# Kernel optimization log

Measured on AMD Instinct MI355X. Metric: run time of the kernel, lower is better.

Reference implementation:

```python
import jax, jax.numpy as jnp
import numpy as np

TEMP = 0.07
W00 = 0.1
EPS = 1e-8


def setup_inputs() -> dict:
    key = jax.random.key(0)
    k1, k2, k3, k4 = jax.random.split(key, 4)
    B, N, D = 32, 256, 256
    M = B * N
    return {
        "audio_feats": jax.random.normal(k1, (B, N, D), dtype=jnp.float32),
        "visual_feats": jax.random.normal(k2, (B, N, D), dtype=jnp.float32),
        "audio_labels": jax.random.randint(k3, (M,), 0, 2, dtype=jnp.int64)
            if jax.config.jax_enable_x64 else jax.random.randint(k3, (M,), 0, 2, dtype=jnp.int32),
        "visual_labels": jax.random.randint(k4, (M,), 0, 2, dtype=jnp.int64)
            if jax.config.jax_enable_x64 else jax.random.randint(k4, (M,), 0, 2, dtype=jnp.int32),
    }


def reference(audio_feats, visual_feats, audio_labels, visual_labels):
    B, N, D = audio_feats.shape
    M = B * N
    a = audio_feats.reshape(M, D)
    v = visual_feats.reshape(M, D)
    # L2 normalize (torch F.normalize uses eps=1e-12 clamp on norm)
    a = a / jnp.maximum(jnp.linalg.norm(a, axis=-1, keepdims=True), 1e-12)
    v = v / jnp.maximum(jnp.linalg.norm(v, axis=-1, keepdims=True), 1e-12)
    sim = (a @ v.T) / TEMP  # (M, M)
    exp_sim = jnp.exp(sim)
    la = audio_labels[:, None]  # (M, 1)
    lv = visual_labels[None, :]  # (1, M)
    pos_mask = (la == lv) & ((la == 1) | (la == 0))
    weight = jnp.where(la == 1, 1.0, W00) * pos_mask.astype(sim.dtype)  # (M, M)
    wexp = exp_sim * weight

    # audio -> visual (row direction)
    denom_a2v = exp_sim.sum(axis=1)
    num_a2v = wexp.sum(axis=1)
    frac_a2v = (num_a2v + EPS) / (denom_a2v + EPS)
    valid_a2v = (num_a2v > 0).astype(sim.dtype)
    loss_a2v = -(valid_a2v * jnp.log(frac_a2v)).sum() / jnp.maximum(valid_a2v.sum(), 1.0)

    # visual -> audio (column direction)
    denom_v2a = exp_sim.sum(axis=0)
    num_v2a = wexp.sum(axis=0)
    frac_v2a = (num_v2a + EPS) / (denom_v2a + EPS)
    valid_v2a = (num_v2a > 0).astype(sim.dtype)
    loss_v2a = -(valid_v2a * jnp.log(frac_v2a)).sum() / jnp.maximum(valid_v2a.sum(), 1.0)

    return 0.5 * (loss_a2v + loss_v2a)
```

## Files before the change

kernel.cpp:

```cpp
#include <hip/hip_runtime.h>

#define M_ROWS 8192
#define D_DIM  256
#define BM     128
#define BN     64
#define NBI    (M_ROWS / BM)
#define NBJ    (M_ROWS / BN)
#define NJOBS  (NBI * NBJ)

#define ALPHA  4.53982478f


typedef __attribute__((ext_vector_type(4))) float floatx4;
typedef __attribute__((ext_vector_type(8))) int   intx8;

__device__ inline float fast_exp2(float x) {
#if __has_builtin(__builtin_amdgcn_exp2f)
    return __builtin_amdgcn_exp2f(x);
#else
    return exp2f(x);
#endif
}

__device__ inline floatx4 mfma_fp8(intx8 a, intx8 b, floatx4 c) {
    return __builtin_amdgcn_mfma_scale_f32_16x16x128_f8f6f4(
        a, b, c, 0, 0, 0, 0x7f7f7f7f, 0, 0x7f7f7f7f);
}

__global__ __launch_bounds__(256) void normalize_kernel(
    const float* __restrict__ af, const float* __restrict__ vf,
    unsigned char* __restrict__ aB, unsigned char* __restrict__ vB,
    float* __restrict__ glob)
{
    __shared__ float ssb[16][4];

    if (blockIdx.x == 0) {
        if (threadIdx.x < 4) glob[threadIdx.x] = 0.f;
        if (threadIdx.x == 4) ((int*)glob)[4] = 0;
    }

    const int b = blockIdx.x;
    const bool isA = b < 512;
    const int T = isA ? b : b - 512;
    const float* src = (isA ? af : vf) + (size_t)T * 16 * D_DIM;
    unsigned char* dst = (isA ? aB : vB) + (size_t)T * 4096;

    const int t    = threadIdx.x;
    const int wave = t >> 6, lane = t & 63;
    const int row  = t & 15;
    const int kq   = (t >> 4) & 3;
    const int h    = (t >> 6) & 1;
    const int s    = t >> 7;
    const int kbase = s * 128 + kq * 32 + h * 16;

    const float* p = src + row * D_DIM + kbase;
    float4 x0 = ((const float4*)p)[0], x1 = ((const float4*)p)[1];
    float4 x2 = ((const float4*)p)[2], x3 = ((const float4*)p)[3];

    float ss = x0.x*x0.x + x0.y*x0.y + x0.z*x0.z + x0.w*x0.w
             + x1.x*x1.x + x1.y*x1.y + x1.z*x1.z + x1.w*x1.w
             + x2.x*x2.x + x2.y*x2.y + x2.z*x2.z + x2.w*x2.w
             + x3.x*x3.x + x3.y*x3.y + x3.z*x3.z + x3.w*x3.w;
    ss += __shfl_xor(ss, 16, 64);
    ss += __shfl_xor(ss, 32, 64);
    if (lane < 16) ssb[lane][wave] = ss;
    __syncthreads();
    float tot = ssb[row][0] + ssb[row][1] + ssb[row][2] + ssb[row][3];
    float scale = ALPHA / fmaxf(sqrtf(tot), 1e-12f);

    int4 o;
    int pk;
    pk  = __builtin_amdgcn_cvt_pk_fp8_f32(x0.x*scale, x0.y*scale, 0, false);
    pk  = __builtin_amdgcn_cvt_pk_fp8_f32(x0.z*scale, x0.w*scale, pk, true);
    o.x = pk;
    pk  = __builtin_amdgcn_cvt_pk_fp8_f32(x1.x*scale, x1.y*scale, 0, false);
    pk  = __builtin_amdgcn_cvt_pk_fp8_f32(x1.z*scale, x1.w*scale, pk, true);
    o.y = pk;
    pk  = __builtin_amdgcn_cvt_pk_fp8_f32(x2.x*scale, x2.y*scale, 0, false);
    pk  = __builtin_amdgcn_cvt_pk_fp8_f32(x2.z*scale, x2.w*scale, pk, true);
    o.z = pk;
    pk  = __builtin_amdgcn_cvt_pk_fp8_f32(x3.x*scale, x3.y*scale, 0, false);
    pk  = __builtin_amdgcn_cvt_pk_fp8_f32(x3.z*scale, x3.w*scale, pk, true);
    o.w = pk;
    *(int4*)(dst + (size_t)t * 16) = o;
}

__global__ __launch_bounds__(256, 4) void gemm_loss_kernel(
    const unsigned char* __restrict__ aB, const unsigned char* __restrict__ vB,
    const int* __restrict__ la, const int* __restrict__ lv,
    float* __restrict__ rowPart, float* __restrict__ colPart)
{
    __shared__ unsigned char ldsB[16384];
    __shared__ float rowbuf[2 * BM];
    __shared__ float colbuf[8 * BN];

    const int tid  = threadIdx.x;
    const int wave = tid >> 6, lane = tid & 63;
    const int quad = lane >> 4, l16 = lane & 15;

    const int bx = blockIdx.x & 63;
    const int by = blockIdx.x >> 6;
    const int i0 = bx * BM, j0 = by * BN;

    {
        const unsigned char* vsrc = vB + (size_t)by * 16384 + (size_t)tid * 16;
        unsigned char* ldst = ldsB + tid * 16;
        #pragma unroll
        for (int c = 0; c < 4; ++c)
            *(int4*)(ldst + c * 4096) = *(const int4*)(vsrc + c * 4096);
    }

    const unsigned char* Abase = aB + (size_t)(bx * 8 + wave * 2) * 4096
                                    + (size_t)lane * 16;
    intx8 afr[2][2];
    #pragma unroll
    for (int it = 0; it < 2; ++it) {
        #pragma unroll
        for (int s = 0; s < 2; ++s) {
            int4 h0 = *(const int4*)(Abase + it * 4096 + s * 2048);
            int4 h1 = *(const int4*)(Abase + it * 4096 + s * 2048 + 1024);
            afr[it][s] = intx8{h0.x, h0.y, h0.z, h0.w, h1.x, h1.y, h1.z, h1.w};
        }
    }

    __syncthreads();

    floatx4 acc[2][4] = {};
    const unsigned char* Bl = ldsB + lane * 16;
    #pragma unroll
    for (int s = 0; s < 2; ++s) {
        #pragma unroll
        for (int jt = 0; jt < 4; ++jt) {
            int4 h0 = *(const int4*)(Bl + jt * 4096 + s * 2048);
            int4 h1 = *(const int4*)(Bl + jt * 4096 + s * 2048 + 1024);
            intx8 bf = intx8{h0.x, h0.y, h0.z, h0.w, h1.x, h1.y, h1.z, h1.w};
            acc[0][jt] = mfma_fp8(afr[0][s], bf, acc[0][jt]);
            acc[1][jt] = mfma_fp8(afr[1][s], bf, acc[1][jt]);
        }
    }

    const int baseRow = i0 + wave * 32;
    float maf[2][4];
    #pragma unroll
    for (int it = 0; it < 2; ++it)
        #pragma unroll
        for (int r = 0; r < 4; ++r)
            maf[it][r] = (float)la[baseRow + it * 16 + quad * 4 + r];
    float mvf[4];
    #pragma unroll
    for (int jt = 0; jt < 4; ++jt)
        mvf[jt] = (float)lv[j0 + jt * 16 + l16];

    float rT[2][4] = {}, r1[2][4] = {};
    float cT[4] = {}, c1[4] = {};
    #pragma unroll
    for (int it = 0; it < 2; ++it) {
        #pragma unroll
        for (int jt = 0; jt < 4; ++jt) {
            #pragma unroll
            for (int r = 0; r < 4; ++r) {
                float e = fast_exp2(acc[it][jt][r]);
                rT[it][r] += e;
                r1[it][r] = fmaf(mvf[jt], e, r1[it][r]);
                cT[jt] += e;
                c1[jt] = fmaf(maf[it][r], e, c1[jt]);
            }
        }
    }

    #pragma unroll
    for (int jt = 0; jt < 4; ++jt) {
        float t0 = cT[jt], t1 = c1[jt];
        t0 += __shfl_xor(t0, 16, 64); t0 += __shfl_xor(t0, 32, 64);
        t1 += __shfl_xor(t1, 16, 64); t1 += __shfl_xor(t1, 32, 64);
        cT[jt] = t0; c1[jt] = t1;
    }

    #pragma unroll
    for (int it = 0; it < 2; ++it) {
        #pragma unroll
        for (int r = 0; r < 4; ++r) {
            float s0 = rT[it][r], s1 = r1[it][r];
            #pragma unroll
            for (int m = 1; m < 16; m <<= 1) {
                s0 += __shfl_xor(s0, m, 64);
                s1 += __shfl_xor(s1, m, 64);
            }
            if (l16 == 0) {
                int rl = wave * 32 + it * 16 + quad * 4 + r;
                rowbuf[rl * 2 + 0] = s0;
                rowbuf[rl * 2 + 1] = s1;
            }
        }
    }
    if (quad == 0) {
        #pragma unroll
        for (int jt = 0; jt < 4; ++jt) {
            colbuf[(wave * 2 + 0) * BN + jt * 16 + l16] = cT[jt];
            colbuf[(wave * 2 + 1) * BN + jt * 16 + l16] = c1[jt];
        }
    }
    __syncthreads();

    {
        const int rl  = tid >> 1;
        const int cls = tid & 1;
        rowPart[((size_t)by * M_ROWS + i0 + rl) * 2 + cls] = rowbuf[rl * 2 + cls];
        if (tid < 128) {
            const int cl = tid >> 1;
            float s = 0.f;
            #pragma unroll
            for (int w = 0; w < 4; ++w)
                s += colbuf[(w * 2 + cls) * BN + cl];
            colPart[((size_t)bx * M_ROWS + j0 + cl) * 2 + cls] = s;
        }
    }
}

__global__ __launch_bounds__(256) void reduce_kernel(
    const float* __restrict__ rowPart, const float* __restrict__ colPart,
    const int* __restrict__ la, const int* __restrict__ lv,
    float* __restrict__ glob, float* __restrict__ out)
{
    const int bid = blockIdx.x;
    const bool aside = bid < 32;
    const int idx = (aside ? bid : bid - 32) * 256 + threadIdx.x;
    const float* part = aside ? rowPart : colPart;
    const int* lab = aside ? la : lv;
    const int nslab = aside ? NBJ : NBI;

    float tot = 0.f, c1 = 0.f;
    #pragma unroll 4
    for (int b = 0; b < nslab; ++b) {
        float2 p = *(const float2*)(part + ((size_t)b * M_ROWS + idx) * 2);
        tot += p.x; c1 += p.y;
    }
    float num = lab[idx] ? c1 : 0.1f * (tot - c1);
    float lg = 0.f, cnt = 0.f;
    if (num > 0.f) { lg = logf((num + 1e-8f) / (tot + 1e-8f)); cnt = 1.f; }

    #pragma unroll
    for (int m = 1; m < 64; m <<= 1) {
        lg  += __shfl_xor(lg,  m, 64);
        cnt += __shfl_xor(cnt, m, 64);
    }
    __shared__ float red[4][2];
    const int w = threadIdx.x >> 6, ln = threadIdx.x & 63;
    if (ln == 0) { red[w][0] = lg; red[w][1] = cnt; }
    __syncthreads();
    if (threadIdx.x == 0) {
        float slg  = red[0][0] + red[1][0] + red[2][0] + red[3][0];
        float scnt = red[0][1] + red[1][1] + red[2][1] + red[3][1];
        float* base = glob + (aside ? 0 : 2);
        atomicAdd(&base[0], slg);
        atomicAdd(&base[1], scnt);
        __threadfence();
        int old = atomicAdd((int*)glob + 4, 1);
        if (old == 63) {
            __threadfence();
            float sA = atomicAdd(&glob[0], 0.f);
            float cA = atomicAdd(&glob[1], 0.f);
            float sV = atomicAdd(&glob[2], 0.f);
            float cV = atomicAdd(&glob[3], 0.f);
            float lossA = -sA / fmaxf(cA, 1.f);
            float lossV = -sV / fmaxf(cV, 1.f);
            out[0] = 0.5f * (lossA + lossV);
        }
    }
}

extern "C" void kernel_launch(void* const* d_in, const int* in_sizes, int n_in,
                              void* d_out, int out_size, void* d_ws, size_t ws_size,
                              hipStream_t stream)
{
    const float* af = (const float*)d_in[0];
    const float* vf = (const float*)d_in[1];
    const int*   la = (const int*)d_in[2];
    const int*   lv = (const int*)d_in[3];
    float* out = (float*)d_out;

    char* ws = (char*)d_ws;
    unsigned char* aB = (unsigned char*)ws;
    unsigned char* vB = (unsigned char*)(ws + 2ull * 1024 * 1024);
    float* rowPart   = (float*)(ws +  4ull * 1024 * 1024);
    float* colPart   = (float*)(ws + 12ull * 1024 * 1024);
    float* glob      = (float*)(ws + 16ull * 1024 * 1024);

    normalize_kernel<<<1024, 256, 0, stream>>>(af, vf, aB, vB, glob);
    gemm_loss_kernel<<<NJOBS, 256, 0, stream>>>(aB, vB, la, lv, rowPart, colPart);
    reduce_kernel<<<64, 256, 0, stream>>>(rowPart, colPart, la, lv, glob, out);
}
```

Measured before the change: 129.1 us.

## Load B tile via global_load_lds and reduce rows through LDS with packed math

The B-operand tile is now loaded with direct global-to-LDS loads instead of going through registers. The epilogue accumulates row and column sums as packed float2 FMAs with a constant 1 lane. Row sums are no longer reduced with a 16-lane shuffle tree; each lane's partials are written into the reused LDS buffer and summed with vector LDS reads. This is meant to cut VGPR traffic, shuffle count and epilogue instructions, at the cost of an extra barrier and more LDS traffic.

```diff
diff --git a/kernel.cpp b/kernel.cpp
--- a/kernel.cpp
+++ b/kernel.cpp
@@ -12,7 +12,13 @@
 
 
 typedef __attribute__((ext_vector_type(4))) float floatx4;
+typedef __attribute__((ext_vector_type(2))) float floatx2;
 typedef __attribute__((ext_vector_type(8))) int   intx8;
+
+#define GLOAD_LDS16(gp, lp) \
+    __builtin_amdgcn_global_load_lds( \
+        (__attribute__((address_space(1))) void*)(gp), \
+        (__attribute__((address_space(3))) void*)(lp), 16, 0, 0)
 
 __device__ inline float fast_exp2(float x) {
 #if __has_builtin(__builtin_amdgcn_exp2f)
@@ -90,9 +96,8 @@
     const int* __restrict__ la, const int* __restrict__ lv,
     float* __restrict__ rowPart, float* __restrict__ colPart)
 {
-    __shared__ unsigned char ldsB[16384];
-    __shared__ float rowbuf[2 * BM];
-    __shared__ float colbuf[8 * BN];
+    __shared__ __align__(16) unsigned char ldsB[16384];
+    __shared__ floatx2 colbuf[4][BN];
 
     const int tid  = threadIdx.x;
     const int wave = tid >> 6, lane = tid & 63;
@@ -107,7 +112,7 @@
         unsigned char* ldst = ldsB + tid * 16;
         #pragma unroll
         for (int c = 0; c < 4; ++c)
-            *(int4*)(ldst + c * 4096) = *(const int4*)(vsrc + c * 4096);
+            GLOAD_LDS16(vsrc + c * 4096, ldst + c * 4096);
     }
 
     const unsigned char* Abase = aB + (size_t)(bx * 8 + wave * 2) * 4096
@@ -140,19 +145,19 @@
     }
 
     const int baseRow = i0 + wave * 32;
-    float maf[2][4];
+    floatx2 ma2[2][4];
     #pragma unroll
     for (int it = 0; it < 2; ++it)
         #pragma unroll
         for (int r = 0; r < 4; ++r)
-            maf[it][r] = (float)la[baseRow + it * 16 + quad * 4 + r];
-    float mvf[4];
+            ma2[it][r] = floatx2{1.f, (float)la[baseRow + it * 16 + quad * 4 + r]};
+    floatx2 mr2[4];
     #pragma unroll
     for (int jt = 0; jt < 4; ++jt)
-        mvf[jt] = (float)lv[j0 + jt * 16 + l16];
-
-    float rT[2][4] = {}, r1[2][4] = {};
-    float cT[4] = {}, c1[4] = {};
+        mr2[jt] = floatx2{1.f, (float)lv[j0 + jt * 16 + l16]};
+
+    floatx2 rowacc[2][4] = {};
+    floatx2 colacc[4] = {};
     #pragma unroll
     for (int it = 0; it < 2; ++it) {
         #pragma unroll
@@ -160,59 +165,48 @@
             #pragma unroll
             for (int r = 0; r < 4; ++r) {
                 float e = fast_exp2(acc[it][jt][r]);
-                rT[it][r] += e;
-                r1[it][r] = fmaf(mvf[jt], e, r1[it][r]);
-                cT[jt] += e;
-                c1[jt] = fmaf(maf[it][r], e, c1[jt]);
+                floatx2 e2 = {e, e};
+                rowacc[it][r] = e2 * mr2[jt] + rowacc[it][r];
+                colacc[jt]   = e2 * ma2[it][r] + colacc[jt];
             }
         }
     }
 
+    __syncthreads();
+
+    floatx2* rp = (floatx2*)ldsB;
+    #pragma unroll
+    for (int it = 0; it < 2; ++it)
+        #pragma unroll
+        for (int r = 0; r < 4; ++r)
+            rp[(wave * 32 + it * 16 + quad * 4 + r) * 16 + l16] = rowacc[it][r];
+
     #pragma unroll
     for (int jt = 0; jt < 4; ++jt) {
-        float t0 = cT[jt], t1 = c1[jt];
-        t0 += __shfl_xor(t0, 16, 64); t0 += __shfl_xor(t0, 32, 64);
-        t1 += __shfl_xor(t1, 16, 64); t1 += __shfl_xor(t1, 32, 64);
-        cT[jt] = t0; c1[jt] = t1;
-    }
-
-    #pragma unroll
-    for (int it = 0; it < 2; ++it) {
-        #pragma unroll
-        for (int r = 0; r < 4; ++r) {
-            float s0 = rT[it][r], s1 = r1[it][r];
-            #pragma unroll
-            for (int m = 1; m < 16; m <<= 1) {
-                s0 += __shfl_xor(s0, m, 64);
-                s1 += __shfl_xor(s1, m, 64);
-            }
-            if (l16 == 0) {
-                int rl = wave * 32 + it * 16 + quad * 4 + r;
-                rowbuf[rl * 2 + 0] = s0;
-                rowbuf[rl * 2 + 1] = s1;
-            }
-        }
-    }
-    if (quad == 0) {
-        #pragma unroll
-        for (int jt = 0; jt < 4; ++jt) {
-            colbuf[(wave * 2 + 0) * BN + jt * 16 + l16] = cT[jt];
-            colbuf[(wave * 2 + 1) * BN + jt * 16 + l16] = c1[jt];
-        }
+        floatx2 v = colacc[jt];
+        v.x += __shfl_xor(v.x, 16, 64); v.y += __shfl_xor(v.y, 16, 64);
+        v.x += __shfl_xor(v.x, 32, 64); v.y += __shfl_xor(v.y, 32, 64);
+        if (quad == 0) colbuf[wave][jt * 16 + l16] = v;
     }
     __syncthreads();
 
     {
-        const int rl  = tid >> 1;
-        const int cls = tid & 1;
-        rowPart[((size_t)by * M_ROWS + i0 + rl) * 2 + cls] = rowbuf[rl * 2 + cls];
-        if (tid < 128) {
-            const int cl = tid >> 1;
-            float s = 0.f;
-            #pragma unroll
-            for (int w = 0; w < 4; ++w)
-                s += colbuf[(w * 2 + cls) * BN + cl];
-            colPart[((size_t)bx * M_ROWS + j0 + cl) * 2 + cls] = s;
+        const int row = tid >> 1, h = tid & 1;
+        const float4* b4 = (const float4*)(rp + (size_t)row * 16 + h * 8);
+        float4 q0 = b4[0], q1 = b4[1], q2 = b4[2], q3 = b4[3];
+        floatx2 s = floatx2{q0.x, q0.y} + floatx2{q0.z, q0.w}
+                  + floatx2{q1.x, q1.y} + floatx2{q1.z, q1.w}
+                  + floatx2{q2.x, q2.y} + floatx2{q2.z, q2.w}
+                  + floatx2{q3.x, q3.y} + floatx2{q3.z, q3.w};
+        s.x += __shfl_xor(s.x, 1, 64);
+        s.y += __shfl_xor(s.y, 1, 64);
+        if (h == 0)
+            *(floatx2*)&rowPart[((size_t)by * M_ROWS + i0 + row) * 2] = s;
+
+        if (tid < BN) {
+            floatx2 c = colbuf[0][tid] + colbuf[1][tid]
+                      + colbuf[2][tid] + colbuf[3][tid];
+            *(floatx2*)&colPart[((size_t)bx * M_ROWS + j0 + tid) * 2] = c;
         }
     }
 }
```

New measurement: 116.4 us. 9.8% less time.
